# Kernel optimization log

Hardware: AMD Instinct MI355X
Metric: run time of the kernel (lower is better)

The kernel has to match this reference:

```python
import jax, jax.numpy as jnp
import numpy as np

D_MODEL = 1024
N_HEADS = 16
D_HEAD = D_MODEL // N_HEADS


def setup_inputs() -> dict:
    key = jax.random.key(0)
    kx, kq, kk, kv = jax.random.split(key, 4)
    B, T = 2, 2048
    X = jax.random.normal(kx, (B, T, D_MODEL), dtype=jnp.float32)
    s = 1.0 / np.sqrt(D_MODEL)
    # torch nn.Linear weight is [out, in]; y = x @ W.T
    Wq = jax.random.uniform(kq, (D_MODEL, D_MODEL), jnp.float32, -s, s)
    Wk = jax.random.uniform(kk, (D_MODEL, D_MODEL), jnp.float32, -s, s)
    Wv = jax.random.uniform(kv, (D_MODEL, D_MODEL), jnp.float32, -s, s)
    return {"X": X, "Wq": Wq, "Wk": Wk, "Wv": Wv}


def reference(X, Wq, Wk, Wv):
    B, T, _ = X.shape
    def heads(W):
        # x @ W.T -> [B,T,D] -> [B,H,T,Dh]
        return (X @ W.T).reshape(B, T, N_HEADS, D_HEAD).transpose(0, 2, 1, 3)
    Q, K, V = heads(Wq), heads(Wk), heads(Wv)
    scores = jnp.einsum('bhqd,bhkd->bhqk', Q, K)
    causal = jnp.tril(jnp.ones((T, T), dtype=bool))
    # original masks with -inf BEFORE scaling; -inf/scale == -inf, so equivalent
    scores = jnp.where(causal, scores, -jnp.inf) / jnp.sqrt(jnp.float32(D_HEAD))
    attn = jax.nn.softmax(scores, axis=-1)
    out = jnp.einsum('bhqk,bhkd->bhqd', attn, V)
    return out.transpose(0, 2, 1, 3).reshape(B, T, N_HEADS * D_HEAD)
```

## Files before the change

### kernel.cpp

```cpp
#include <hip/hip_runtime.h>


using bf16x8  = __attribute__((ext_vector_type(8))) __bf16;
using floatx4 = __attribute__((ext_vector_type(4))) float;

#define T_SEQ   2048
#define D_MODEL 1024
#define N_HEADS 16
#define D_HEAD  64
#define BATCH   2
#define M_TOT   4096
#define N_TOT   3072
#define PLANE   (T_SEQ * D_HEAD)
#define NX      (M_TOT * D_MODEL)
#define NWSEG   (D_MODEL * D_MODEL)
#define QSCALE  0.18033688f
#define SM_BIAS 24.0f

__device__ __forceinline__ unsigned short f32_to_bf16(float f) {
  unsigned int u = __float_as_uint(f);
  u += 0x7fffu + ((u >> 16) & 1u);
  return (unsigned short)(u >> 16);
}
__device__ __forceinline__ unsigned int pack2_bf16(float a, float b) {
  unsigned int ua = __float_as_uint(a) + 0x8000u;
  unsigned int ub = __float_as_uint(b) + 0x8000u;
  return __builtin_amdgcn_perm(ub, ua, 0x07060302);
}
__device__ __forceinline__ void async_cp16(void* lds, const void* gptr) {
  __builtin_amdgcn_global_load_lds(
      (const __attribute__((address_space(1))) unsigned int*)gptr,
      (__attribute__((address_space(3))) unsigned int*)lds, 16, 0, 0);
}

__global__ __launch_bounds__(256) void cvt_kernel(
    const float* __restrict__ X,  const float* __restrict__ Wq,
    const float* __restrict__ Wk, const float* __restrict__ Wv,
    unsigned short* __restrict__ Xb, unsigned short* __restrict__ Wb)
{
  const size_t i = ((size_t)blockIdx.x * 256 + threadIdx.x) * 8;
  const float* src;
  unsigned short* dst;
  if (i < NX) { src = X + i; dst = Xb + i; }
  else {
    const size_t r = i - NX;
    const int w = (int)(r >> 20);
    const size_t o = r & (NWSEG - 1);
    src = ((w == 0) ? Wq : (w == 1) ? Wk : Wv) + o;
    dst = Wb + r;
  }
  float4 f0 = *(const float4*)src;
  float4 f1 = *(const float4*)(src + 4);
  uint4 out;
  out.x = pack2_bf16(f0.x, f0.y);
  out.y = pack2_bf16(f0.z, f0.w);
  out.z = pack2_bf16(f1.x, f1.y);
  out.w = pack2_bf16(f1.z, f1.w);
  *(uint4*)dst = out;
}

__global__ __launch_bounds__(256) void gemm_qkv(
    const unsigned short* __restrict__ Xb,
    const unsigned short* __restrict__ Wb,
    unsigned short* __restrict__ Qb,
    unsigned short* __restrict__ Kb,
    unsigned short* __restrict__ VTb)
{
  __shared__ unsigned short Als[128 * 64];
  __shared__ unsigned short Bls[128 * 64];

  const int tid  = threadIdx.x;
  const int lane = tid & 63;
  const int wave = tid >> 6;
  const int l15  = lane & 15;
  const int quad = lane >> 4;
  const int wm   = wave >> 1, wn = wave & 1;

  const int n_blk = blockIdx.x * 128;
  const int m_blk = blockIdx.y * 128;

  const int swz = (((tid >> 3) ^ tid) & 7) * 8;
  const unsigned short* Ag = Xb + (size_t)(m_blk + (tid >> 3)) * D_MODEL + swz;
  const unsigned short* Bg = Wb + (size_t)(n_blk + (tid >> 3)) * D_MODEL + swz;
  char* Alds = (char*)Als + wave * 1024;
  char* Blds = (char*)Bls + wave * 1024;

  floatx4 acc[4][4] = {};

  for (int k0 = 0; k0 < D_MODEL; k0 += 64) {
    __syncthreads();
#pragma unroll
    for (int p = 0; p < 4; p++) {
      async_cp16(Alds + p * 4096, Ag + (size_t)p * 32 * D_MODEL + k0);
      async_cp16(Blds + p * 4096, Bg + (size_t)p * 32 * D_MODEL + k0);
    }
    __syncthreads();

#pragma unroll
    for (int ks = 0; ks < 2; ks++) {
      bf16x8 a[4], b[4];
#pragma unroll
      for (int i = 0; i < 4; i++) {
        const int sa = ((ks * 4 + quad) ^ (l15 & 7)) * 16;
        a[i] = *(const bf16x8*)((char*)Als + (wm * 64 + 16 * i + l15) * 128 + sa);
        b[i] = *(const bf16x8*)((char*)Bls + (wn * 64 + 16 * i + l15) * 128 + sa);
      }
#pragma unroll
      for (int mi = 0; mi < 4; mi++)
#pragma unroll
        for (int ni = 0; ni < 4; ni++)
          acc[mi][ni] = __builtin_amdgcn_mfma_f32_16x16x32_bf16(a[mi], b[ni], acc[mi][ni], 0, 0, 0);
    }
  }

  __syncthreads();
  char* ep = (char*)Als + wave * 8192;
  const int w_sel  = n_blk >> 10;
  const int m_base = m_blk + wm * 64;
  const int n_base = n_blk + wn * 64;
  const int h      = (n_base & 1023) >> 6;
  const float csc  = (w_sel == 0) ? QSCALE : 1.0f;

  if (w_sel < 2) {
#pragma unroll
    for (int mi = 0; mi < 4; mi++)
#pragma unroll
      for (int ni = 0; ni < 4; ni++)
#pragma unroll
        for (int r = 0; r < 4; r++) {
          const int row  = 16 * mi + quad * 4 + r;
          const int colb = (16 * ni + l15) * 2;
          const int phys = ((colb >> 4) ^ (row & 7)) * 16;
          *(unsigned short*)(ep + row * 128 + phys + (colb & 15)) =
              f32_to_bf16(acc[mi][ni][r] * csc);
        }
  } else {
#pragma unroll
    for (int mi = 0; mi < 4; mi++)
#pragma unroll
      for (int ni = 0; ni < 4; ni++)
#pragma unroll
        for (int r = 0; r < 4; r++) {
          const int row  = 16 * ni + l15;
          const int colb = (16 * mi + quad * 4 + r) * 2;
          const int phys = ((colb >> 4) ^ (row & 7)) * 16;
          *(unsigned short*)(ep + row * 128 + phys + (colb & 15)) =
              f32_to_bf16(acc[mi][ni][r]);
        }
  }
  asm volatile("s_waitcnt lgkmcnt(0)" ::: "memory");

#pragma unroll
  for (int pass = 0; pass < 8; pass++) {
    const int row  = pass * 8 + (lane >> 3);
    const int phys = ((lane & 7) ^ (row & 7)) * 16;
    uint4 v = *(const uint4*)(ep + row * 128 + phys);
    if (w_sel < 2) {
      const int m  = m_base + row;
      const int bb = m >> 11;
      const int t  = m & (T_SEQ - 1);
      unsigned short* dst = ((w_sel == 0) ? Qb : Kb) +
          ((size_t)(bb * N_HEADS + h) * T_SEQ + t) * D_HEAD + (lane & 7) * 8;
      *(uint4*)dst = v;
    } else {
      const int bb = m_base >> 11;
      unsigned short* dst = VTb +
          ((size_t)(bb * N_HEADS + h) * D_HEAD + row) * T_SEQ + (m_base & (T_SEQ - 1)) + (lane & 7) * 8;
      *(uint4*)dst = v;
    }
  }
}

__global__ __launch_bounds__(256) void attn_kernel(
    const unsigned short* __restrict__ Qb,
    const unsigned short* __restrict__ Kb,
    const unsigned short* __restrict__ VTb,
    float* __restrict__ Out)
{
  __shared__ unsigned short Ks[2][64 * 64];
  __shared__ unsigned short Vs[2][64 * 64];
  __shared__ unsigned short Ps[4][16 * 64];

  const int tid  = threadIdx.x;
  const int lane = tid & 63;
  const int wave = tid >> 6;
  const int l15  = lane & 15;
  const int quad = lane >> 4;

  const int bh    = blockIdx.x & 31;
  const int strip = 31 - (blockIdx.x >> 5);
  const int q0w   = strip * 64 + wave * 16;
  const int nch   = strip + 1;

  const unsigned short* Qp = Qb  + (size_t)bh * PLANE;
  const unsigned short* Kp = Kb  + (size_t)bh * PLANE;
  const unsigned short* Vp = VTb + (size_t)bh * PLANE;

  const int swz = (((tid >> 3) ^ tid) & 7) * 8;
  const unsigned short* Kg = Kp + (size_t)(tid >> 3) * D_HEAD + swz;
  const unsigned short* Vg = Vp + (size_t)(tid >> 3) * T_SEQ + swz;
  unsigned short* myp = Ps[wave];
  const int b = bh >> 4, h = bh & 15;

  bf16x8 aq[2];
#pragma unroll
  for (int s = 0; s < 2; s++)
    aq[s] = *(const bf16x8*)(Qp + (size_t)(q0w + l15) * D_HEAD + 32 * s + quad * 8);

  float l_acc[4] = {};
  floatx4 o[4] = {};

#pragma unroll
  for (int p = 0; p < 2; p++) {
    async_cp16((char*)Ks[0] + p * 4096 + wave * 1024, Kg + (size_t)(p * 32) * D_HEAD);
    async_cp16((char*)Vs[0] + p * 4096 + wave * 1024, Vg + (size_t)(p * 32) * T_SEQ);
  }

  for (int jc = 0; jc < nch; jc++) {
    __syncthreads();
    if (jc + 1 < nch) {
      const int j1 = (jc + 1) * 64;
      char* kd = (char*)Ks[(jc + 1) & 1];
      char* vd = (char*)Vs[(jc + 1) & 1];
#pragma unroll
      for (int p = 0; p < 2; p++) {
        async_cp16(kd + p * 4096 + wave * 1024, Kg + (size_t)(j1 + p * 32) * D_HEAD);
        async_cp16(vd + p * 4096 + wave * 1024, Vg + (size_t)(p * 32) * T_SEQ + j1);
      }
    }
    const char* Ksb = (const char*)Ks[jc & 1];
    const char* Vsb = (const char*)Vs[jc & 1];

    floatx4 s[4] = {};
#pragma unroll
    for (int t = 0; t < 4; t++)
#pragma unroll
      for (int ss = 0; ss < 2; ss++) {
        const int sa = ((ss * 4 + quad) ^ (l15 & 7)) * 16;
        bf16x8 bk = *(const bf16x8*)(Ksb + (16 * t + l15) * 128 + sa);
        s[t] = __builtin_amdgcn_mfma_f32_16x16x32_bf16(aq[ss], bk, s[t], 0, 0, 0);
      }

    if (jc == nch - 1) {
      const int j0 = jc * 64;
#pragma unroll
      for (int t = 0; t < 4; t++) {
        const int kk = j0 + 16 * t + l15;
#pragma unroll
        for (int r = 0; r < 4; r++)
          if (kk > q0w + quad * 4 + r) s[t][r] = -INFINITY;
      }
    }

#pragma unroll
    for (int t = 0; t < 4; t++)
#pragma unroll
      for (int r = 0; r < 4; r++)
        s[t][r] = exp2f(s[t][r] - SM_BIAS);
#pragma unroll
    for (int r = 0; r < 4; r++)
      l_acc[r] += (s[0][r] + s[1][r]) + (s[2][r] + s[3][r]);

#pragma unroll
    for (int t = 0; t < 4; t++)
#pragma unroll
      for (int r = 0; r < 4; r++) {
        const int row  = quad * 4 + r;
        const int phys = ((2 * t + (l15 >> 3)) ^ (row & 7)) * 16;
        *(unsigned short*)((char*)myp + row * 128 + phys + (l15 & 7) * 2) =
            f32_to_bf16(s[t][r]);
      }
    asm volatile("s_waitcnt lgkmcnt(0)" ::: "memory");

#pragma unroll
    for (int ks = 0; ks < 2; ks++) {
      const int pa = ((ks * 4 + quad) ^ (l15 & 7)) * 16;
      bf16x8 ap = *(const bf16x8*)((char*)myp + l15 * 128 + pa);
#pragma unroll
      for (int n = 0; n < 4; n++) {
        const int sa = ((ks * 4 + quad) ^ (l15 & 7)) * 16;
        bf16x8 bv = *(const bf16x8*)(Vsb + (16 * n + l15) * 128 + sa);
        o[n] = __builtin_amdgcn_mfma_f32_16x16x32_bf16(ap, bv, o[n], 0, 0, 0);
      }
    }
  }

#pragma unroll
  for (int r = 0; r < 4; r++) {
#pragma unroll
    for (int d = 1; d < 16; d <<= 1) l_acc[r] += __shfl_xor(l_acc[r], d);
  }

#pragma unroll
  for (int r = 0; r < 4; r++) {
    const float inv_l = 1.0f / l_acc[r];
    const int t = q0w + quad * 4 + r;
#pragma unroll
    for (int n = 0; n < 4; n++)
      Out[(size_t)(b * T_SEQ + t) * D_MODEL + h * D_HEAD + 16 * n + l15] = o[n][r] * inv_l;
  }
}

extern "C" void kernel_launch(void* const* d_in, const int* in_sizes, int n_in,
                              void* d_out, int out_size, void* d_ws, size_t ws_size,
                              hipStream_t stream) {
  const float* X  = (const float*)d_in[0];
  const float* Wq = (const float*)d_in[1];
  const float* Wk = (const float*)d_in[2];
  const float* Wv = (const float*)d_in[3];

  unsigned short* Qb = (unsigned short*)d_ws;
  unsigned short* Kb = Qb + (size_t)BATCH * N_HEADS * T_SEQ * D_HEAD;
  unsigned short* VT = Kb + (size_t)BATCH * N_HEADS * T_SEQ * D_HEAD;

  unsigned short* Xb = (unsigned short*)d_out;
  unsigned short* Wb = Xb + (size_t)NX;

  cvt_kernel<<<3584, 256, 0, stream>>>(X, Wq, Wk, Wv, Xb, Wb);

  dim3 g1(N_TOT / 128, M_TOT / 128);
  gemm_qkv<<<g1, 256, 0, stream>>>(Xb, Wb, Qb, Kb, VT);

  attn_kernel<<<1024, 256, 0, stream>>>(Qb, Kb, VT, (float*)d_out);
}
```

Before: 161.3 us.

## Transpose QK^T MFMA output, pack P stores, and interleave causal strip order

Swaps the MFMA operands so each lane holds four consecutive keys for one query row. This lets P be converted with packed bf16 instructions and written as one 8-byte LDS store per tile instead of sixteen 2-byte stores. The row sum becomes a single per-lane accumulator reduced with two shuffles, and the exp uses the raw hardware builtin. Block-to-strip mapping now interleaves short and long causal strips to balance load across CUs. The trade-offs are an extra shuffle per output row and a dependency on inline asm for the bf16 conversion.

```diff
diff --git a/kernel.cpp b/kernel.cpp
--- a/kernel.cpp
+++ b/kernel.cpp
@@ -187,10 +187,14 @@
   const int l15  = lane & 15;
   const int quad = lane >> 4;
 
-  const int bh    = blockIdx.x & 31;
-  const int strip = 31 - (blockIdx.x >> 5);
-  const int q0w   = strip * 64 + wave * 16;
-  const int nch   = strip + 1;
+  const int bh   = blockIdx.x & 31;
+  const int slot = blockIdx.x >> 5;
+  const int x    = slot & 7;
+  const int pos  = slot >> 3;
+  const int strip = (pos == 0) ? x : (pos == 1) ? (15 - x)
+                  : (pos == 2) ? (16 + x) : (31 - x);
+  const int q0w  = strip * 64 + wave * 16;
+  const int nch  = strip + 1;
 
   const unsigned short* Qp = Qb  + (size_t)bh * PLANE;
   const unsigned short* Kp = Kb  + (size_t)bh * PLANE;
@@ -199,7 +203,7 @@
   const int swz = (((tid >> 3) ^ tid) & 7) * 8;
   const unsigned short* Kg = Kp + (size_t)(tid >> 3) * D_HEAD + swz;
   const unsigned short* Vg = Vp + (size_t)(tid >> 3) * T_SEQ + swz;
-  unsigned short* myp = Ps[wave];
+  char* myp = (char*)Ps[wave];
   const int b = bh >> 4, h = bh & 15;
 
   bf16x8 aq[2];
@@ -207,7 +211,7 @@
   for (int s = 0; s < 2; s++)
     aq[s] = *(const bf16x8*)(Qp + (size_t)(q0w + l15) * D_HEAD + 32 * s + quad * 8);
 
-  float l_acc[4] = {};
+  float l_lane = 0.0f;
   floatx4 o[4] = {};
 
 #pragma unroll
@@ -238,17 +242,18 @@
       for (int ss = 0; ss < 2; ss++) {
         const int sa = ((ss * 4 + quad) ^ (l15 & 7)) * 16;
         bf16x8 bk = *(const bf16x8*)(Ksb + (16 * t + l15) * 128 + sa);
-        s[t] = __builtin_amdgcn_mfma_f32_16x16x32_bf16(aq[ss], bk, s[t], 0, 0, 0);
+        s[t] = __builtin_amdgcn_mfma_f32_16x16x32_bf16(bk, aq[ss], s[t], 0, 0, 0);
       }
 
     if (jc == nch - 1) {
       const int j0 = jc * 64;
+      const int q  = q0w + l15;
 #pragma unroll
       for (int t = 0; t < 4; t++) {
-        const int kk = j0 + 16 * t + l15;
+        const int kb = j0 + 16 * t + quad * 4;
 #pragma unroll
         for (int r = 0; r < 4; r++)
-          if (kk > q0w + quad * 4 + r) s[t][r] = -INFINITY;
+          if (kb + r > q) s[t][r] = -INFINITY;
       }
     }
 
@@ -256,26 +261,25 @@
     for (int t = 0; t < 4; t++)
 #pragma unroll
       for (int r = 0; r < 4; r++)
-        s[t][r] = exp2f(s[t][r] - SM_BIAS);
-#pragma unroll
-    for (int r = 0; r < 4; r++)
-      l_acc[r] += (s[0][r] + s[1][r]) + (s[2][r] + s[3][r]);
-
+        s[t][r] = __builtin_amdgcn_exp2f(s[t][r] - SM_BIAS);
 #pragma unroll
     for (int t = 0; t < 4; t++)
-#pragma unroll
-      for (int r = 0; r < 4; r++) {
-        const int row  = quad * 4 + r;
-        const int phys = ((2 * t + (l15 >> 3)) ^ (row & 7)) * 16;
-        *(unsigned short*)((char*)myp + row * 128 + phys + (l15 & 7) * 2) =
-            f32_to_bf16(s[t][r]);
-      }
+      l_lane += (s[t][0] + s[t][1]) + (s[t][2] + s[t][3]);
+
+#pragma unroll
+    for (int t = 0; t < 4; t++) {
+      uint2 w;
+      asm("v_cvt_pk_bf16_f32 %0, %1, %2" : "=v"(w.x) : "v"(s[t][0]), "v"(s[t][1]));
+      asm("v_cvt_pk_bf16_f32 %0, %1, %2" : "=v"(w.y) : "v"(s[t][2]), "v"(s[t][3]));
+      const int phys = (((2 * t + (quad >> 1)) ^ (l15 & 7)) * 16) + 8 * (quad & 1);
+      *(uint2*)(myp + l15 * 128 + phys) = w;
+    }
     asm volatile("s_waitcnt lgkmcnt(0)" ::: "memory");
 
 #pragma unroll
     for (int ks = 0; ks < 2; ks++) {
       const int pa = ((ks * 4 + quad) ^ (l15 & 7)) * 16;
-      bf16x8 ap = *(const bf16x8*)((char*)myp + l15 * 128 + pa);
+      bf16x8 ap = *(const bf16x8*)(myp + l15 * 128 + pa);
 #pragma unroll
       for (int n = 0; n < 4; n++) {
         const int sa = ((ks * 4 + quad) ^ (l15 & 7)) * 16;
@@ -285,15 +289,12 @@
     }
   }
 
+  l_lane += __shfl_xor(l_lane, 16);
+  l_lane += __shfl_xor(l_lane, 32);
+
 #pragma unroll
   for (int r = 0; r < 4; r++) {
-#pragma unroll
-    for (int d = 1; d < 16; d <<= 1) l_acc[r] += __shfl_xor(l_acc[r], d);
-  }
-
-#pragma unroll
-  for (int r = 0; r < 4; r++) {
-    const float inv_l = 1.0f / l_acc[r];
+    const float inv_l = 1.0f / __shfl(l_lane, quad * 4 + r);
     const int t = q0w + quad * 4 + r;
 #pragma unroll
     for (int n = 0; n < 4; n++)
```

New measurement: 154.4 us. -4.2%, faster.
